# Performance work log

Hardware: AMD Instinct MI355X
Metric: run time of the kernel (lower is better)

Reference implementation:

```python
import jax, jax.numpy as jnp
import numpy as np

# ---- dims / hyperparams (match init_kwargs) ----
D, B, S, NE, NC = 256, 4, 8192, 2048, 512
WIN, RK, TKE, TKC = 4, 4, 4, 4          # s window, route_topk, expanded_topk, compressed_topk
ALPHA, BS2B, BB2S = 1.0, 0.5, 0.5       # alpha_b, beta_s_to_b, beta_b_to_s
S_SC, B_SC, X_SC = 0.25, 0.2, 0.15      # s/b/cross delta scales
EPS = 1e-5
INV_SQRT_D = float(1.0 / np.sqrt(D))


def _ln(x, g, b):
    m = jnp.mean(x, -1, keepdims=True)
    v = jnp.mean(jnp.square(x - m), -1, keepdims=True)
    return (x - m) * jax.lax.rsqrt(v + EPS) * g + b


def _window_prop(state, val, w):
    # local window attention via diagonal-bilinear pairwise scores; never builds [S,S]
    n = state.shape[1]
    offs = jnp.arange(-WIN, WIN + 1)
    idx = jnp.arange(n)[:, None] + offs[None, :]            # [n, K]
    valid = (idx >= 0) & (idx < n)
    idxc = jnp.clip(idx, 0, n - 1)
    nb_s = state[:, idxc]                                    # [B, n, K, D]
    nb_v = val[:, idxc]
    sc = jnp.einsum('bnd,bnkd->bnk', state * w, nb_s) * INV_SQRT_D
    sc = jnp.where(valid, sc, -1e30)
    a = jax.nn.softmax(sc, axis=-1)
    return (jnp.einsum('bnk,bnkd->bnd', a, nb_s),
            jnp.einsum('bnk,bnkd->bnd', a, nb_v))


def _topk_prop(state, val, w, k):
    # global topk sparse attention over the (small) expanded/compressed node set
    sc = jnp.einsum('bnd,bmd->bnm', state * w, state) * INV_SQRT_D
    top, idx = jax.lax.top_k(sc, k)                          # [B, N, k]
    a = jax.nn.softmax(top, axis=-1)
    take = jax.vmap(lambda x, i: x[i])                       # gather rows per batch
    nb_s = take(state, idx)                                  # [B, N, k, D]
    nb_v = take(val, idx)
    return (jnp.einsum('bnk,bnkd->bnd', a, nb_s),
            jnp.einsum('bnk,bnkd->bnd', a, nb_v))


def _sparse_transition(src_s, src_v, W, bias, nd, k):
    # LinearRoute logits -> topk dst per src -> softmax weights -> scatter-add into dst
    logits = src_s @ W + bias                                # [B, Ns, Nd]
    top, idx = jax.lax.top_k(logits, k)
    wgt = jax.nn.softmax(top, axis=-1)                       # [B, Ns, k]

    def scat(i, ww, fs, fv):
        ii = i.reshape(-1)
        cs = (ww[..., None] * fs[:, None, :]).reshape(-1, fs.shape[-1])
        cv = (ww[..., None] * fv[:, None, :]).reshape(-1, fv.shape[-1])
        z = jnp.zeros((nd, fs.shape[-1]), fs.dtype)
        return z.at[ii].add(cs), z.at[ii].add(cv)

    return jax.vmap(scat)(idx, wgt, src_s, src_v)            # [B, Nd, D] x2


def _forward(s_state, s_val, w_pair_s, w_pair_e, w_pair_c,
             W_expand, b_expand, W_b2s, b_b2s, W_comp, b_comp, W_s2b, b_s2b,
             ln_g_s, ln_b_s, ln_g_e, ln_b_e, ln_g_c, ln_b_c):
    bsz = s_state.shape[0]
    # 1) sequence window propagation + stabilize
    ds, dv = _window_prop(s_state, s_val, w_pair_s)
    s_state = jnp.tanh(s_state + S_SC * ds)
    s_val = _ln(s_val + S_SC * dv, ln_g_s, ln_b_s)
    # 2) compressed layer bootstrapped from zeros (compressed_b=None) + stabilize
    c_state = jnp.zeros((bsz, NC, D), s_state.dtype)
    c_val = _ln(jnp.zeros((bsz, NC, D), s_state.dtype), ln_g_c, ln_b_c)
    # 3) expanded layer: expand transition then topk propagation + stabilize
    e_state = jnp.zeros((bsz, NE, D), s_state.dtype)
    e_val = jnp.zeros((bsz, NE, D), s_state.dtype)
    sc_b = ALPHA * B_SC
    ds, dv = _sparse_transition(c_state, c_val, W_expand, b_expand, NE, RK)
    e_state = e_state + sc_b * ds; e_val = e_val + sc_b * dv
    ds, dv = _topk_prop(e_state, e_val, w_pair_e, TKE)
    e_state = jnp.tanh(e_state + sc_b * ds)
    e_val = _ln(e_val + sc_b * dv, ln_g_e, ln_b_e)
    # 4) expanded -> sequence cross update + stabilize
    sc_x = ALPHA * BB2S * X_SC
    ds, dv = _sparse_transition(e_state, e_val, W_b2s, b_b2s, S, RK)
    s_state = jnp.tanh(s_state + sc_x * ds)
    s_val = _ln(s_val + sc_x * dv, ln_g_s, ln_b_s)
    # 5) next compressed: compress, s->b, compressed propagation + stabilize
    nc_state, nc_val = c_state, c_val
    ds, dv = _sparse_transition(e_state, e_val, W_comp, b_comp, NC, RK)
    nc_state = nc_state + sc_b * ds; nc_val = nc_val + sc_b * dv
    sc_sb = ALPHA * BS2B * X_SC
    ds, dv = _sparse_transition(s_state, s_val, W_s2b, b_s2b, NC, RK)
    nc_state = nc_state + sc_sb * ds; nc_val = nc_val + sc_sb * dv
    ds, dv = _topk_prop(nc_state, nc_val, w_pair_c, TKC)
    nc_state = jnp.tanh(nc_state + sc_b * ds)
    nc_val = _ln(nc_val + sc_b * dv, ln_g_c, ln_b_c)
    return (s_state, s_val, nc_state, nc_val)


def setup_inputs() -> dict:
    key = jax.random.key(0)
    ks = jax.random.split(key, 16)
    rs = float(1.0 / np.sqrt(D))
    return {
        's_state': jax.random.normal(ks[0], (B, S, D), jnp.float32),
        's_val': jax.random.normal(ks[1], (B, S, D), jnp.float32),
        'w_pair_s': jax.random.normal(ks[2], (D,), jnp.float32) * rs,
        'w_pair_e': jax.random.normal(ks[3], (D,), jnp.float32) * rs,
        'w_pair_c': jax.random.normal(ks[4], (D,), jnp.float32) * rs,
        'W_expand': jax.random.normal(ks[5], (D, NE), jnp.float32) * rs,
        'b_expand': jnp.zeros((NE,), jnp.float32),
        'W_b2s': jax.random.normal(ks[6], (D, S), jnp.float32) * rs,
        'b_b2s': jnp.zeros((S,), jnp.float32),
        'W_comp': jax.random.normal(ks[7], (D, NC), jnp.float32) * rs,
        'b_comp': jnp.zeros((NC,), jnp.float32),
        'W_s2b': jax.random.normal(ks[8], (D, NC), jnp.float32) * rs,
        'b_s2b': jnp.zeros((NC,), jnp.float32),
        'ln_g_s': jnp.ones((D,), jnp.float32), 'ln_b_s': jnp.zeros((D,), jnp.float32),
        'ln_g_e': jnp.ones((D,), jnp.float32), 'ln_b_e': jnp.zeros((D,), jnp.float32),
        'ln_g_c': jnp.ones((D,), jnp.float32), 'ln_b_c': jnp.zeros((D,), jnp.float32),
    }


def reference(s_state, s_val, w_pair_s, w_pair_e, w_pair_c,
              W_expand, b_expand, W_b2s, b_b2s, W_comp, b_comp, W_s2b, b_s2b,
              ln_g_s, ln_b_s, ln_g_e, ln_b_e, ln_g_c, ln_b_c):
    return _forward(s_state, s_val, w_pair_s, w_pair_e, w_pair_c,
                    W_expand, b_expand, W_b2s, b_b2s, W_comp, b_comp, W_s2b, b_s2b,
                    ln_g_s, ln_b_s, ln_g_e, ln_b_e, ln_g_c, ln_b_c)
```

## Files before the change

kernel.cpp:

```cpp
#include <hip/hip_runtime.h>
#include <math.h>

#define DD 256
#define BATCH 4
#define SEQ 8192
#define NEE 2048
#define NCC 512
#define EPSL 1e-5f
#define INV_SQRT_D 0.0625f

typedef __attribute__((ext_vector_type(8))) short short8;
typedef __attribute__((ext_vector_type(4))) float f32x4;

__device__ __forceinline__ float4 ld4(const float* p){ return *(const float4*)p; }
__device__ __forceinline__ void st4(float* p, const float4& v){ *(float4*)p = v; }
__device__ __forceinline__ void fma4(float4& a, float s, const float4& b){
  a.x = fmaf(s,b.x,a.x); a.y = fmaf(s,b.y,a.y); a.z = fmaf(s,b.z,a.z); a.w = fmaf(s,b.w,a.w);
}
__device__ __forceinline__ float4 tanh4(const float4& v){
  float4 r; r.x=tanhf(v.x); r.y=tanhf(v.y); r.z=tanhf(v.z); r.w=tanhf(v.w); return r;
}
__device__ __forceinline__ ushort f2bf(float x){
  unsigned u = __float_as_uint(x);
  unsigned r = u + 0x7fffu + ((u >> 16) & 1u);
  return (ushort)(r >> 16);
}
__device__ __forceinline__ float bf2f(ushort h){
  return __uint_as_float(((unsigned)h) << 16);
}

__device__ __forceinline__ bool t4_better(float v1, int i1, float v2, int i2){
  return (v1 > v2) || (v1 == v2 && i1 < i2);
}
__device__ __forceinline__ void t4_init(float* v, int* i){
#pragma unroll
  for (int k=0;k<4;k++){ v[k] = -INFINITY; i[k] = 0x7fffffff; }
}
__device__ __forceinline__ void t4_insert(float* v, int* i, float nv, int ni){
  if (t4_better(nv, ni, v[3], i[3])){
    v[3]=nv; i[3]=ni;
    if (t4_better(v[3],i[3],v[2],i[2])){ float tv=v[2]; v[2]=v[3]; v[3]=tv; int ti=i[2]; i[2]=i[3]; i[3]=ti;
      if (t4_better(v[2],i[2],v[1],i[1])){ tv=v[1]; v[1]=v[2]; v[2]=tv; ti=i[1]; i[1]=i[2]; i[2]=ti;
        if (t4_better(v[1],i[1],v[0],i[0])){ tv=v[0]; v[0]=v[1]; v[1]=tv; ti=i[0]; i[0]=i[1]; i[1]=ti; }
      }
    }
  }
}
__device__ __forceinline__ void t4_ce(float* v, int* i, int x, int y){
  if (t4_better(v[y],i[y],v[x],i[x])){ float tv=v[x]; v[x]=v[y]; v[y]=tv; int ti=i[x]; i[x]=i[y]; i[y]=ti; }
}
__device__ __forceinline__ void t4_merge(float* av, int* ai, const float* bv, const int* bi){
  float lv[4]; int li[4];
#pragma unroll
  for (int k=0;k<4;k++){
    if (t4_better(av[k],ai[k],bv[3-k],bi[3-k])){ lv[k]=av[k]; li[k]=ai[k]; }
    else { lv[k]=bv[3-k]; li[k]=bi[3-k]; }
  }
  t4_ce(lv,li,0,2); t4_ce(lv,li,1,3); t4_ce(lv,li,0,1); t4_ce(lv,li,2,3);
#pragma unroll
  for (int k=0;k<4;k++){ av[k]=lv[k]; ai[k]=li[k]; }
}
__device__ __forceinline__ void t4_wave_merge(float* v, int* i){
#pragma unroll
  for (int off=1; off<64; off<<=1){
    float bv[4]; int bi[4];
#pragma unroll
    for (int k=0;k<4;k++){ bv[k]=__shfl_xor(v[k],off); bi[k]=__shfl_xor(i[k],off); }
    t4_merge(v,i,bv,bi);
  }
}

__global__ __launch_bounds__(256) void k0_prep(
    const float* __restrict__ b_expand, const float* __restrict__ b_b2s, const float* __restrict__ b_comp,
    const float* __restrict__ ln_b_c, const float* __restrict__ ln_g_e, const float* __restrict__ ln_b_e,
    float* __restrict__ sumE, int* __restrict__ idxB2S, float* __restrict__ wgtB2S,
    int* __restrict__ idxComp, float* __restrict__ wgtComp)
{
  __shared__ int s_idx[3][4];
  __shared__ float s_wgt[3][4];
  __shared__ float red[16];
  int t = threadIdx.x, wv = t>>6, lane = t&63;
  if (wv < 3){
    const float* arr = (wv==0)? b_expand : (wv==1? b_b2s : b_comp);
    int n = (wv==0)? NEE : (wv==1? SEQ : NCC);
    float v[4]; int ix[4]; t4_init(v,ix);
    for (int m=lane; m<n; m+=64) t4_insert(v,ix, arr[m], m);
    t4_wave_merge(v,ix);
    if (lane==0){
      float e0=1.f, e1=expf(v[1]-v[0]), e2=expf(v[2]-v[0]), e3=expf(v[3]-v[0]);
      float inv = 1.f/(e0+e1+e2+e3);
      s_idx[wv][0]=ix[0]; s_idx[wv][1]=ix[1]; s_idx[wv][2]=ix[2]; s_idx[wv][3]=ix[3];
      s_wgt[wv][0]=e0*inv; s_wgt[wv][1]=e1*inv; s_wgt[wv][2]=e2*inv; s_wgt[wv][3]=e3*inv;
    }
  }
  __syncthreads();
  float c = ln_b_c[t];
  float cs = c, cq = c*c;
#pragma unroll
  for (int off=32; off; off>>=1){ cs += __shfl_xor(cs,off); cq += __shfl_xor(cq,off); }
  if (lane==0){ red[wv]=cs; red[8+wv]=cq; }
  __syncthreads();
  float mean_c = (red[0]+red[1]+red[2]+red[3]) * (1.f/256.f);
  float var_c  = (red[8]+red[9]+red[10]+red[11]) * (1.f/256.f) - mean_c*mean_c;
  float cm = c - mean_c;
  float g = ln_g_e[t], be = ln_b_e[t];
  float a[4]; float q = 0.f;
#pragma unroll
  for (int k=0;k<4;k++){
    a[k] = 0.2f * (float)NCC * s_wgt[0][k];
    if (s_idx[0][k] < 4) q += a[k];
  }
  q *= 0.25f;
  float se = 0.f;
#pragma unroll
  for (int k=0;k<4;k++){
    float tk = a[k] + 0.2f*q;
    se += tk*cm*rsqrtf(tk*tk*var_c + EPSL)*g + be;
  }
  float tz = 0.2f*q;
  se += (float)(NEE-4) * (tz*cm*rsqrtf(tz*tz*var_c + EPSL)*g + be);
  sumE[t] = se;
  if (t < 4){
    idxB2S[t] = s_idx[1][t]; wgtB2S[t] = s_wgt[1][t];
    idxComp[t] = s_idx[2][t]; wgtComp[t] = s_wgt[2][t];
  }
}

__global__ __launch_bounds__(256) void k1_window(
    const float* __restrict__ s_state, const float* __restrict__ s_val,
    const float* __restrict__ w_pair_s, const float* __restrict__ ln_g_s, const float* __restrict__ ln_b_s,
    const float* __restrict__ sumE, const int* __restrict__ idxB2S, const float* __restrict__ wgtB2S,
    float* __restrict__ out_state, float* __restrict__ out_val)
{
  int gw = (blockIdx.x << 2) + (threadIdx.x >> 6);
  int lane = threadIdx.x & 63;
  int b = gw >> 13, r = gw & (SEQ-1);
  size_t rowoff = ((size_t)gw) << 8;
  size_t bbase = ((size_t)b) << 21;
  int d0 = lane << 2;
  float4 x = ld4(s_state + rowoff + d0);
  float4 v = ld4(s_val + rowoff + d0);
  float4 wp = ld4(w_pair_s + d0);
  float qx=x.x*wp.x, qy=x.y*wp.y, qz=x.z*wp.z, qw=x.w*wp.w;
  float sc[9]; float4 ns[9];
#pragma unroll
  for (int k=0;k<9;k++){
    int rr = r + k - 4;
    int rc = rr < 0 ? 0 : (rr > SEQ-1 ? SEQ-1 : rr);
    ns[k] = ld4(s_state + bbase + (((size_t)rc)<<8) + d0);
    sc[k] = qx*ns[k].x + qy*ns[k].y + qz*ns[k].z + qw*ns[k].w;
  }
#pragma unroll
  for (int off=32; off; off>>=1){
#pragma unroll
    for (int k=0;k<9;k++) sc[k] += __shfl_xor(sc[k], off);
  }
  float mx = -INFINITY;
#pragma unroll
  for (int k=0;k<9;k++){
    int rr = r + k - 4;
    sc[k] = (rr>=0 && rr<SEQ) ? sc[k]*INV_SQRT_D : -1e30f;
    mx = fmaxf(mx, sc[k]);
  }
  float ssum = 0.f;
#pragma unroll
  for (int k=0;k<9;k++){ sc[k] = expf(sc[k]-mx); ssum += sc[k]; }
  float inv = 1.f/ssum;
  float4 ds = make_float4(0,0,0,0), dv = make_float4(0,0,0,0);
#pragma unroll
  for (int k=0;k<9;k++) fma4(ds, sc[k]*inv, ns[k]);
#pragma unroll
  for (int k=0;k<9;k++){
    int rr = r + k - 4;
    int rc = rr < 0 ? 0 : (rr > SEQ-1 ? SEQ-1 : rr);
    float4 nv = ld4(s_val + bbase + (((size_t)rc)<<8) + d0);
    fma4(dv, sc[k]*inv, nv);
  }
  float4 s1;
  s1.x = tanhf(x.x + 0.25f*ds.x); s1.y = tanhf(x.y + 0.25f*ds.y);
  s1.z = tanhf(x.z + 0.25f*ds.z); s1.w = tanhf(x.w + 0.25f*ds.w);
  st4(out_state + rowoff + d0, tanh4(s1));
  float4 y;
  y.x = v.x + 0.25f*dv.x; y.y = v.y + 0.25f*dv.y; y.z = v.z + 0.25f*dv.z; y.w = v.w + 0.25f*dv.w;
  float sm = y.x+y.y+y.z+y.w;
  float sq = y.x*y.x+y.y*y.y+y.z*y.z+y.w*y.w;
#pragma unroll
  for (int off=32; off; off>>=1){ sm += __shfl_xor(sm,off); sq += __shfl_xor(sq,off); }
  float mean = sm*(1.f/256.f);
  float rstd = rsqrtf(sq*(1.f/256.f) - mean*mean + EPSL);
  float4 g = ld4(ln_g_s + d0), be = ld4(ln_b_s + d0);
  float4 y1;
  y1.x = (y.x-mean)*rstd*g.x + be.x; y1.y = (y.y-mean)*rstd*g.y + be.y;
  y1.z = (y.z-mean)*rstd*g.z + be.z; y1.w = (y.w-mean)*rstd*g.w + be.w;
#pragma unroll
  for (int k=0;k<4;k++){
    if (r == idxB2S[k]){
      float cb = 0.075f * wgtB2S[k];
      float4 sE = ld4(sumE + d0);
      fma4(y1, cb, sE);
    }
  }
  sm = y1.x+y1.y+y1.z+y1.w;
  sq = y1.x*y1.x+y1.y*y1.y+y1.z*y1.z+y1.w*y1.w;
#pragma unroll
  for (int off=32; off; off>>=1){ sm += __shfl_xor(sm,off); sq += __shfl_xor(sq,off); }
  float mean2 = sm*(1.f/256.f);
  float rstd2 = rsqrtf(sq*(1.f/256.f) - mean2*mean2 + EPSL);
  float4 o;
  o.x = (y1.x-mean2)*rstd2*g.x + be.x; o.y = (y1.y-mean2)*rstd2*g.y + be.y;
  o.z = (y1.z-mean2)*rstd2*g.z + be.z; o.w = (y1.w-mean2)*rstd2*g.w + be.w;
  st4(out_val + rowoff + d0, o);
}

__global__ __launch_bounds__(256) void k2w_pack(const float* __restrict__ W,
    ushort* __restrict__ Whi, ushort* __restrict__ Wlo)
{
  int t = blockIdx.x*256 + threadIdx.x;
  int kb = t >> 11;
  int cf = (t >> 6) & 31;
  int l  = t & 63;
  int k0 = kb*32 + ((l>>4)<<3);
  int col = (cf<<4) + (l&15);
  size_t off = (size_t)t << 3;
#pragma unroll
  for (int j=0;j<8;j++){
    float x = W[(size_t)(k0+j)*NCC + col];
    ushort h = f2bf(x);
    Whi[off+j] = h;
    Wlo[off+j] = f2bf(x - bf2f(h));
  }
}

__global__ __launch_bounds__(256, 4) void k2_mfma(
    const float* __restrict__ A, const ushort* __restrict__ Whi,
    const float* __restrict__ bias,
    int* __restrict__ topk_idx, float* __restrict__ topk_wgt, int* __restrict__ counts)
{
  __shared__ __align__(16) ushort Asp[2][32][264];
  __shared__ float mv[32][17];
  __shared__ int   mi[32][17];
  int tid = threadIdx.x;
  size_t row_base = (size_t)blockIdx.x * 32;
  int w = tid >> 6, l = tid & 63;
  int lg = l >> 4, lr = l & 15;
  const ushort* pw = Whi + ((w<<12) + (l<<3));

#define LOADG(KB, G, DST) { \
    const ushort* _p = pw + (KB)*16384 + (G)*1024; \
    DST[0] = *(const short8*)_p; \
    DST[2] = *(const short8*)(_p + 512); \
    DST[1] = *(const short8*)(_p + 131072); \
    DST[3] = *(const short8*)(_p + 131072 + 512); }

#define COMPG(G, B) { \
    int _c0 = (G)<<1, _c1 = _c0+1; \
    acc[0][_c0] = __builtin_amdgcn_mfma_f32_16x16x32_bf16(ah0, B[0], acc[0][_c0], 0,0,0); \
    acc[1][_c0] = __builtin_amdgcn_mfma_f32_16x16x32_bf16(ah1, B[0], acc[1][_c0], 0,0,0); \
    acc[0][_c1] = __builtin_amdgcn_mfma_f32_16x16x32_bf16(ah0, B[2], acc[0][_c1], 0,0,0); \
    acc[1][_c1] = __builtin_amdgcn_mfma_f32_16x16x32_bf16(ah1, B[2], acc[1][_c1], 0,0,0); \
    acc[0][_c0] = __builtin_amdgcn_mfma_f32_16x16x32_bf16(al0, B[0], acc[0][_c0], 0,0,0); \
    acc[1][_c0] = __builtin_amdgcn_mfma_f32_16x16x32_bf16(al1, B[0], acc[1][_c0], 0,0,0); \
    acc[0][_c0] = __builtin_amdgcn_mfma_f32_16x16x32_bf16(ah0, B[1], acc[0][_c0], 0,0,0); \
    acc[1][_c0] = __builtin_amdgcn_mfma_f32_16x16x32_bf16(ah1, B[1], acc[1][_c0], 0,0,0); \
    acc[0][_c1] = __builtin_amdgcn_mfma_f32_16x16x32_bf16(al0, B[2], acc[0][_c1], 0,0,0); \
    acc[1][_c1] = __builtin_amdgcn_mfma_f32_16x16x32_bf16(al1, B[2], acc[1][_c1], 0,0,0); \
    acc[0][_c1] = __builtin_amdgcn_mfma_f32_16x16x32_bf16(ah0, B[3], acc[0][_c1], 0,0,0); \
    acc[1][_c1] = __builtin_amdgcn_mfma_f32_16x16x32_bf16(ah1, B[3], acc[1][_c1], 0,0,0); }

  short8 bA[4], bB[4];
  LOADG(0, 0, bA);
  {
    const float4* Ab = (const float4*)(A + row_base*DD);
#pragma unroll
    for (int i=0;i<8;i++){
      int q = i*256 + tid;
      int row = q >> 6, k4 = q & 63;
      float4 x = Ab[q];
      ushort4 h, lo;
      h.x = f2bf(x.x); h.y = f2bf(x.y); h.z = f2bf(x.z); h.w = f2bf(x.w);
      lo.x = f2bf(x.x - bf2f(h.x)); lo.y = f2bf(x.y - bf2f(h.y));
      lo.z = f2bf(x.z - bf2f(h.z)); lo.w = f2bf(x.w - bf2f(h.w));
      *(ushort4*)&Asp[0][row][k4*4] = h;
      *(ushort4*)&Asp[1][row][k4*4] = lo;
    }
  }
  __syncthreads();
  f32x4 acc[2][8];
#pragma unroll
  for (int rf=0; rf<2; rf++)
#pragma unroll
    for (int cf=0; cf<8; cf++) acc[rf][cf] = (f32x4){0.f,0.f,0.f,0.f};
#pragma unroll 1
  for (int kb=0; kb<8; kb++){
    int ka = kb*32 + (lg<<3);
    short8 ah0 = *(const short8*)&Asp[0][lr][ka];
    short8 ah1 = *(const short8*)&Asp[0][16+lr][ka];
    short8 al0 = *(const short8*)&Asp[1][lr][ka];
    short8 al1 = *(const short8*)&Asp[1][16+lr][ka];
    LOADG(kb, 1, bB);
    __builtin_amdgcn_sched_barrier(0);
    COMPG(0, bA);
    LOADG(kb, 2, bA);
    __builtin_amdgcn_sched_barrier(0);
    COMPG(1, bB);
    LOADG(kb, 3, bB);
    __builtin_amdgcn_sched_barrier(0);
    COMPG(2, bA);
    if (kb < 7) LOADG(kb+1, 0, bA);
    __builtin_amdgcn_sched_barrier(0);
    COMPG(3, bB);
  }
#undef LOADG
#undef COMPG
  float bcol[8];
  int rel[8];
#pragma unroll
  for (int cf=0; cf<8; cf++){
    bcol[cf] = bias[(w<<7) + (cf<<4) + lr];
    rel[cf] = (cf<<4) + lr;
  }
#pragma unroll
  for (int rf=0; rf<2; rf++){
#pragma unroll
    for (int reg=0; reg<4; reg++){
      float av[8];
#pragma unroll
      for (int cf=0; cf<8; cf++) av[cf] = acc[rf][cf][reg] + bcol[cf];
      float tv4[4]; int tc4[4];
#pragma unroll
      for (int r=0; r<4; r++){
        float m = fmaxf(fmaxf(fmaxf(av[0],av[1]),fmaxf(av[2],av[3])),
                        fmaxf(fmaxf(av[4],av[5]),fmaxf(av[6],av[7])));
#pragma unroll
        for (int off=1; off<16; off<<=1) m = fmaxf(m, __shfl_xor(m, off));
        int cand = 0x7fffffff;
#pragma unroll
        for (int cf=7; cf>=0; cf--) cand = (av[cf]==m) ? rel[cf] : cand;
#pragma unroll
        for (int off=1; off<16; off<<=1) cand = min(cand, __shfl_xor(cand, off));
        tv4[r] = m; tc4[r] = cand;
        if (r < 3){
#pragma unroll
          for (int cf=0; cf<8; cf++) av[cf] = (rel[cf]==cand) ? -INFINITY : av[cf];
        }
      }
      if (lr == 0){
        int rowl = (rf<<4) + (lg<<2) + reg;
#pragma unroll
        for (int r=0; r<4; r++){ mv[rowl][(w<<2)+r] = tv4[r]; mi[rowl][(w<<2)+r] = (w<<7) + tc4[r]; }
      }
    }
  }
  __syncthreads();
  if (tid < 32){
    float v[4]; int ix[4]; t4_init(v, ix);
#pragma unroll
    for (int j=0; j<16; j++) t4_insert(v, ix, mv[tid][j], mi[tid][j]);
    float e0=1.f, e1=expf(v[1]-v[0]), e2=expf(v[2]-v[0]), e3=expf(v[3]-v[0]);
    float inv = 1.f/(e0+e1+e2+e3);
    size_t row = row_base + tid;
    int b = (int)(row >> 13);
    topk_idx[row*4+0]=ix[0]; topk_idx[row*4+1]=ix[1]; topk_idx[row*4+2]=ix[2]; topk_idx[row*4+3]=ix[3];
    topk_wgt[row*4+0]=e0*inv; topk_wgt[row*4+1]=e1*inv; topk_wgt[row*4+2]=e2*inv; topk_wgt[row*4+3]=e3*inv;
    atomicAdd(&counts[(b<<9)+ix[0]],1); atomicAdd(&counts[(b<<9)+ix[1]],1);
    atomicAdd(&counts[(b<<9)+ix[2]],1); atomicAdd(&counts[(b<<9)+ix[3]],1);
  }
}

__global__ void kz_zero(int* __restrict__ counts){
  int i = blockIdx.x*256 + threadIdx.x;
  if (i < BATCH*NCC) counts[i] = 0;
}

__global__ __launch_bounds__(256) void k3_scan(const int* __restrict__ counts,
    int* __restrict__ offsets, int* __restrict__ cursor)
{
  __shared__ int part[256];
  int t = threadIdx.x;
  int loc[8]; int s = 0;
#pragma unroll
  for (int i=0;i<8;i++){ loc[i] = counts[t*8+i]; s += loc[i]; }
  part[t] = s;
  __syncthreads();
  for (int off=1; off<256; off<<=1){
    int add = (t>=off)? part[t-off] : 0;
    __syncthreads();
    part[t] += add;
    __syncthreads();
  }
  int run = part[t] - s;
#pragma unroll
  for (int i=0;i<8;i++){ offsets[t*8+i] = run; cursor[t*8+i] = run; run += loc[i]; }
  if (t==255) offsets[BATCH*NCC] = run;
}

__global__ void k4_fill(const int* __restrict__ topk_idx, const float* __restrict__ topk_wgt,
    int* __restrict__ cursor, int* __restrict__ csr_src, float* __restrict__ csr_wgt)
{
  int row = blockIdx.x*256 + threadIdx.x;
  if (row >= BATCH*SEQ) return;
  int b = row >> 13, r = row & (SEQ-1);
#pragma unroll
  for (int k=0;k<4;k++){
    int dest = topk_idx[row*4+k];
    float wgt = topk_wgt[row*4+k];
    int pos = atomicAdd(&cursor[(b<<9)+dest], 1);
    csr_src[pos] = r;
    csr_wgt[pos] = 0.075f * wgt;
  }
}

__global__ __launch_bounds__(256) void k5_gather(
    const int* __restrict__ offsets, const int* __restrict__ csr_src, const float* __restrict__ csr_wgt,
    const float* __restrict__ st, const float* __restrict__ vl,
    const float* __restrict__ ln_b_c, const float* __restrict__ sumE,
    const int* __restrict__ idxComp, const float* __restrict__ wgtComp,
    float* __restrict__ ncs, float* __restrict__ ncv)
{
  int g = blockIdx.x;
  int b = g >> 9, dest = g & (NCC-1);
  int t = threadIdx.x;
  int i0 = offsets[g], i1 = offsets[g+1];
  const float* Sb = st + (((size_t)b)<<21);
  const float* Vb = vl + (((size_t)b)<<21);
  float accs = 0.f, accv = 0.f;
  for (int i=i0; i<i1; i++){
    int src = csr_src[i];
    float wg = csr_wgt[i];
    accs = fmaf(wg, Sb[((size_t)src<<8) + t], accs);
    accv = fmaf(wg, Vb[((size_t)src<<8) + t], accv);
  }
  float base = ln_b_c[t];
#pragma unroll
  for (int k=0;k<4;k++) if (dest == idxComp[k]) base = fmaf(0.2f*wgtComp[k], sumE[t], base);
  ncs[((size_t)g<<8) + t] = accs;
  ncv[((size_t)g<<8) + t] = base + accv;
}

__global__ __launch_bounds__(256) void k5t_transpose(const float* __restrict__ ncs, float* __restrict__ ncsT){
  __shared__ float tile[64][65];
  int b = blockIdx.z;
  int m0 = blockIdx.x*64, d0 = blockIdx.y*64;
  int tx = threadIdx.x & 63, ty = threadIdx.x >> 6;
  const float* src = ncs + (((size_t)b)<<17);
  for (int i=ty; i<64; i+=4) tile[i][tx] = src[(size_t)(m0+i)*DD + d0 + tx];
  __syncthreads();
  float* dst = ncsT + (((size_t)b)<<17);
  for (int i=ty; i<64; i+=4) dst[(size_t)(d0+i)*NCC + m0 + tx] = tile[tx][i];
}

__global__ __launch_bounds__(256) void k6_ncprop(
    const float* __restrict__ ncs, const float* __restrict__ ncv, const float* __restrict__ ncsT,
    const float* __restrict__ w_pair_c, const float* __restrict__ ln_g_c, const float* __restrict__ ln_b_c,
    float* __restrict__ o_ncs, float* __restrict__ o_ncv)
{
  __shared__ float Alds[256*13];
  int tid = threadIdx.x;
  int b = blockIdx.x >> 6;
  int n_base = (blockIdx.x & 63) << 3;
  const float* Sb = ncs + (((size_t)b)<<17);
  const float* Vb = ncv + (((size_t)b)<<17);
  const float* Tb = ncsT + (((size_t)b)<<17);
  float wc = w_pair_c[tid] * INV_SQRT_D;
#pragma unroll
  for (int i=0;i<8;i++) Alds[tid*13 + i] = Sb[(size_t)(n_base+i)*DD + tid] * wc;
  __syncthreads();
  int lane = tid & 63, rg = tid >> 6;
  int r0 = rg << 1, c0 = lane << 3;
  float acc[2][8];
#pragma unroll
  for (int j=0;j<2;j++)
#pragma unroll
    for (int c=0;c<8;c++) acc[j][c] = 0.f;
  for (int kk=0; kk<256; kk++){
    float4 w0 = ld4(Tb + (size_t)kk*NCC + c0);
    float4 w1 = ld4(Tb + (size_t)kk*NCC + c0 + 4);
    float a0 = Alds[kk*13 + r0];
    float a1 = Alds[kk*13 + r0 + 1];
    float wv_[8] = {w0.x,w0.y,w0.z,w0.w,w1.x,w1.y,w1.z,w1.w};
#pragma unroll
    for (int c=0;c<8;c++){
      acc[0][c] = fmaf(a0, wv_[c], acc[0][c]);
      acc[1][c] = fmaf(a1, wv_[c], acc[1][c]);
    }
  }
  int d0 = lane << 2;
  float4 g4 = ld4(ln_g_c + d0), be4 = ld4(ln_b_c + d0);
#pragma unroll
  for (int j=0;j<2;j++){
    float tv[4]; int ti[4]; t4_init(tv,ti);
#pragma unroll
    for (int c=0;c<8;c++) t4_insert(tv,ti, acc[j][c], c0+c);
    t4_wave_merge(tv,ti);
    float e0=1.f, e1=expf(tv[1]-tv[0]), e2=expf(tv[2]-tv[0]), e3=expf(tv[3]-tv[0]);
    float inv = 1.f/(e0+e1+e2+e3);
    float aw[4] = {e0*inv, e1*inv, e2*inv, e3*inv};
    int n = n_base + r0 + j;
    float4 stt = ld4(Sb + (size_t)n*DD + d0);
    float4 vv  = ld4(Vb + (size_t)n*DD + d0);
    float4 dsv = make_float4(0,0,0,0), dvv = make_float4(0,0,0,0);
#pragma unroll
    for (int k=0;k<4;k++){
      float4 ms = ld4(Sb + (size_t)ti[k]*DD + d0);
      float4 mv = ld4(Vb + (size_t)ti[k]*DD + d0);
      fma4(dsv, aw[k], ms); fma4(dvv, aw[k], mv);
    }
    float4 os;
    os.x = tanhf(stt.x + 0.2f*dsv.x); os.y = tanhf(stt.y + 0.2f*dsv.y);
    os.z = tanhf(stt.z + 0.2f*dsv.z); os.w = tanhf(stt.w + 0.2f*dsv.w);
    size_t orow = (((size_t)b)<<17) + ((size_t)n<<8);
    st4(o_ncs + orow + d0, os);
    float4 y;
    y.x = vv.x + 0.2f*dvv.x; y.y = vv.y + 0.2f*dvv.y;
    y.z = vv.z + 0.2f*dvv.z; y.w = vv.w + 0.2f*dvv.w;
    float sm = y.x+y.y+y.z+y.w;
    float sq = y.x*y.x+y.y*y.y+y.z*y.z+y.w*y.w;
#pragma unroll
    for (int off=32; off; off>>=1){ sm += __shfl_xor(sm,off); sq += __shfl_xor(sq,off); }
    float mean = sm*(1.f/256.f);
    float rstd = rsqrtf(sq*(1.f/256.f) - mean*mean + EPSL);
    float4 o;
    o.x = (y.x-mean)*rstd*g4.x + be4.x; o.y = (y.y-mean)*rstd*g4.y + be4.y;
    o.z = (y.z-mean)*rstd*g4.z + be4.z; o.w = (y.w-mean)*rstd*g4.w + be4.w;
    st4(o_ncv + orow + d0, o);
  }
}

extern "C" void kernel_launch(void* const* d_in, const int* in_sizes, int n_in,
                              void* d_out, int out_size, void* d_ws, size_t ws_size,
                              hipStream_t stream)
{
  const float* s_state = (const float*)d_in[0];
  const float* s_val   = (const float*)d_in[1];
  const float* w_pair_s= (const float*)d_in[2];
  const float* w_pair_c= (const float*)d_in[4];
  const float* b_expand= (const float*)d_in[6];
  const float* b_b2s   = (const float*)d_in[8];
  const float* b_comp  = (const float*)d_in[10];
  const float* W_s2b   = (const float*)d_in[11];
  const float* b_s2b   = (const float*)d_in[12];
  const float* ln_g_s  = (const float*)d_in[13];
  const float* ln_b_s  = (const float*)d_in[14];
  const float* ln_g_e  = (const float*)d_in[15];
  const float* ln_b_e  = (const float*)d_in[16];
  const float* ln_g_c  = (const float*)d_in[17];
  const float* ln_b_c  = (const float*)d_in[18];

  float* o_sstate = (float*)d_out;
  float* o_sval   = o_sstate + (size_t)BATCH*SEQ*DD;
  float* o_ncs    = o_sval + (size_t)BATCH*SEQ*DD;
  float* o_ncv    = o_ncs + (size_t)BATCH*NCC*DD;

  char* w = (char*)d_ws;
  float* sumE    = (float*)(w);
  int*   idxB2S  = (int*)(w + 1024);
  float* wgtB2S  = (float*)(w + 1040);
  int*   idxComp = (int*)(w + 1056);
  float* wgtComp = (float*)(w + 1072);
  int*   topk_idx= (int*)(w + 4096);
  float* topk_wgt= (float*)(w + 4096 + 524288);
  int*   counts  = (int*)(w + 1052672);
  int*   offsets = (int*)(w + 1069056);
  int*   cursor  = (int*)(w + 1085440);
  int*   csr_src = (int*)(w + 1101824);
  float* csr_wgt = (float*)(w + 1626112);
  float* ncs_ws  = (float*)(w + 2150400);
  float* ncv_ws  = ncs_ws + (size_t)BATCH*NCC*DD;
  float* ncsT_ws = ncv_ws + (size_t)BATCH*NCC*DD;
  ushort* wpk_hi = (ushort*)(w + 8441856);
  ushort* wpk_lo = (ushort*)(w + 8441856 + 262144);

  hipLaunchKernelGGL(k0_prep, dim3(1), dim3(256), 0, stream,
      b_expand, b_b2s, b_comp, ln_b_c, ln_g_e, ln_b_e, sumE, idxB2S, wgtB2S, idxComp, wgtComp);
  hipLaunchKernelGGL(k2w_pack, dim3(64), dim3(256), 0, stream, W_s2b, wpk_hi, wpk_lo);
  hipLaunchKernelGGL(k1_window, dim3(8192), dim3(256), 0, stream,
      s_state, s_val, w_pair_s, ln_g_s, ln_b_s, sumE, idxB2S, wgtB2S, o_sstate, o_sval);
  hipLaunchKernelGGL(kz_zero, dim3(8), dim3(256), 0, stream, counts);
  hipLaunchKernelGGL(k2_mfma, dim3(1024), dim3(256), 0, stream,
      o_sstate, wpk_hi, b_s2b, topk_idx, topk_wgt, counts);
  hipLaunchKernelGGL(k3_scan, dim3(1), dim3(256), 0, stream, counts, offsets, cursor);
  hipLaunchKernelGGL(k4_fill, dim3(128), dim3(256), 0, stream,
      topk_idx, topk_wgt, cursor, csr_src, csr_wgt);
  hipLaunchKernelGGL(k5_gather, dim3(2048), dim3(256), 0, stream,
      offsets, csr_src, csr_wgt, o_sstate, o_sval, ln_b_c, sumE, idxComp, wgtComp, ncs_ws, ncv_ws);
  hipLaunchKernelGGL(k5t_transpose, dim3(8,4,BATCH), dim3(256), 0, stream, ncs_ws, ncsT_ws);
  hipLaunchKernelGGL(k6_ncprop, dim3(256), dim3(256), 0, stream,
      ncs_ws, ncv_ws, ncsT_ws, w_pair_c, ln_g_c, ln_b_c, o_ncs, o_ncv);
}
```

Before: 420.0 us.

## Split CSR gather across two blocks per destination with atomic accumulation

The gather kernel now launches two blocks per compressed destination, each handling half of the source list, and adds partial sums into pre-initialized buffers with float atomics. A new init kernel zeroes the accumulators, writes the bias base and zeroes the counts, replacing the old zero kernel. The inner loop is unrolled by four with independent accumulators so more gathered loads are in flight. This targets load imbalance and latency in the gather, at the cost of an extra init pass, atomic traffic and nondeterministic summation order.

```diff
diff --git a/kernel.cpp b/kernel.cpp
--- a/kernel.cpp
+++ b/kernel.cpp
@@ -123,6 +123,26 @@
   if (t < 4){
     idxB2S[t] = s_idx[1][t]; wgtB2S[t] = s_wgt[1][t];
     idxComp[t] = s_idx[2][t]; wgtComp[t] = s_wgt[2][t];
+  }
+}
+
+__global__ __launch_bounds__(256) void kz_init(int* __restrict__ counts,
+    float* __restrict__ ncs, float* __restrict__ ncv,
+    const float* __restrict__ ln_b_c, const float* __restrict__ sumE,
+    const int* __restrict__ idxComp, const float* __restrict__ wgtComp)
+{
+  int bid = blockIdx.x;
+  int t = threadIdx.x;
+  if (bid < BATCH*NCC){
+    int dest = bid & (NCC-1);
+    float base = ln_b_c[t];
+#pragma unroll
+    for (int k=0;k<4;k++) if (dest == idxComp[k]) base = fmaf(0.2f*wgtComp[k], sumE[t], base);
+    ncs[((size_t)bid<<8) + t] = 0.f;
+    ncv[((size_t)bid<<8) + t] = base;
+  } else {
+    int i = (bid - BATCH*NCC)*256 + t;
+    if (i < BATCH*NCC) counts[i] = 0;
   }
 }
 
@@ -367,11 +387,6 @@
   }
 }
 
-__global__ void kz_zero(int* __restrict__ counts){
-  int i = blockIdx.x*256 + threadIdx.x;
-  if (i < BATCH*NCC) counts[i] = 0;
-}
-
 __global__ __launch_bounds__(256) void k3_scan(const int* __restrict__ counts,
     int* __restrict__ offsets, int* __restrict__ cursor)
 {
@@ -413,28 +428,45 @@
 __global__ __launch_bounds__(256) void k5_gather(
     const int* __restrict__ offsets, const int* __restrict__ csr_src, const float* __restrict__ csr_wgt,
     const float* __restrict__ st, const float* __restrict__ vl,
-    const float* __restrict__ ln_b_c, const float* __restrict__ sumE,
-    const int* __restrict__ idxComp, const float* __restrict__ wgtComp,
     float* __restrict__ ncs, float* __restrict__ ncv)
 {
-  int g = blockIdx.x;
-  int b = g >> 9, dest = g & (NCC-1);
+  int g2 = blockIdx.x;
+  int g  = g2 >> 1;
+  int half = g2 & 1;
+  int b = g >> 9;
   int t = threadIdx.x;
   int i0 = offsets[g], i1 = offsets[g+1];
+  int n = i1 - i0;
+  int ia = i0 + ((n * half) >> 1);
+  int ib = i0 + ((n * (half+1)) >> 1);
+  if (ia >= ib) return;
   const float* Sb = st + (((size_t)b)<<21);
   const float* Vb = vl + (((size_t)b)<<21);
-  float accs = 0.f, accv = 0.f;
-  for (int i=i0; i<i1; i++){
+  float as0=0.f, as1=0.f, as2=0.f, as3=0.f;
+  float av0=0.f, av1=0.f, av2=0.f, av3=0.f;
+  int i = ia;
+  for (; i+3 < ib; i += 4){
+    int s0 = csr_src[i],   s1 = csr_src[i+1], s2 = csr_src[i+2], s3 = csr_src[i+3];
+    float w0 = csr_wgt[i], w1 = csr_wgt[i+1], w2 = csr_wgt[i+2], w3 = csr_wgt[i+3];
+    float x0 = Sb[((size_t)s0<<8)+t], y0 = Vb[((size_t)s0<<8)+t];
+    float x1 = Sb[((size_t)s1<<8)+t], y1 = Vb[((size_t)s1<<8)+t];
+    float x2 = Sb[((size_t)s2<<8)+t], y2 = Vb[((size_t)s2<<8)+t];
+    float x3 = Sb[((size_t)s3<<8)+t], y3 = Vb[((size_t)s3<<8)+t];
+    as0 = fmaf(w0,x0,as0); av0 = fmaf(w0,y0,av0);
+    as1 = fmaf(w1,x1,as1); av1 = fmaf(w1,y1,av1);
+    as2 = fmaf(w2,x2,as2); av2 = fmaf(w2,y2,av2);
+    as3 = fmaf(w3,x3,as3); av3 = fmaf(w3,y3,av3);
+  }
+  for (; i < ib; i++){
     int src = csr_src[i];
     float wg = csr_wgt[i];
-    accs = fmaf(wg, Sb[((size_t)src<<8) + t], accs);
-    accv = fmaf(wg, Vb[((size_t)src<<8) + t], accv);
-  }
-  float base = ln_b_c[t];
-#pragma unroll
-  for (int k=0;k<4;k++) if (dest == idxComp[k]) base = fmaf(0.2f*wgtComp[k], sumE[t], base);
-  ncs[((size_t)g<<8) + t] = accs;
-  ncv[((size_t)g<<8) + t] = base + accv;
+    as0 = fmaf(wg, Sb[((size_t)src<<8)+t], as0);
+    av0 = fmaf(wg, Vb[((size_t)src<<8)+t], av0);
+  }
+  float accs = (as0+as1)+(as2+as3);
+  float accv = (av0+av1)+(av2+av3);
+  atomicAdd(&ncs[((size_t)g<<8) + t], accs);
+  atomicAdd(&ncv[((size_t)g<<8) + t], accv);
 }
 
 __global__ __launch_bounds__(256) void k5t_transpose(const float* __restrict__ ncs, float* __restrict__ ncsT){
@@ -572,17 +604,18 @@
 
   hipLaunchKernelGGL(k0_prep, dim3(1), dim3(256), 0, stream,
       b_expand, b_b2s, b_comp, ln_b_c, ln_g_e, ln_b_e, sumE, idxB2S, wgtB2S, idxComp, wgtComp);
+  hipLaunchKernelGGL(kz_init, dim3(BATCH*NCC + 8), dim3(256), 0, stream,
+      counts, ncs_ws, ncv_ws, ln_b_c, sumE, idxComp, wgtComp);
   hipLaunchKernelGGL(k2w_pack, dim3(64), dim3(256), 0, stream, W_s2b, wpk_hi, wpk_lo);
   hipLaunchKernelGGL(k1_window, dim3(8192), dim3(256), 0, stream,
       s_state, s_val, w_pair_s, ln_g_s, ln_b_s, sumE, idxB2S, wgtB2S, o_sstate, o_sval);
-  hipLaunchKernelGGL(kz_zero, dim3(8), dim3(256), 0, stream, counts);
   hipLaunchKernelGGL(k2_mfma, dim3(1024), dim3(256), 0, stream,
       o_sstate, wpk_hi, b_s2b, topk_idx, topk_wgt, counts);
   hipLaunchKernelGGL(k3_scan, dim3(1), dim3(256), 0, stream, counts, offsets, cursor);
   hipLaunchKernelGGL(k4_fill, dim3(128), dim3(256), 0, stream,
       topk_idx, topk_wgt, cursor, csr_src, csr_wgt);
-  hipLaunchKernelGGL(k5_gather, dim3(2048), dim3(256), 0, stream,
-      offsets, csr_src, csr_wgt, o_sstate, o_sval, ln_b_c, sumE, idxComp, wgtComp, ncs_ws, ncv_ws);
+  hipLaunchKernelGGL(k5_gather, dim3(4096), dim3(256), 0, stream,
+      offsets, csr_src, csr_wgt, o_sstate, o_sval, ncs_ws, ncv_ws);
   hipLaunchKernelGGL(k5t_transpose, dim3(8,4,BATCH), dim3(256), 0, stream, ncs_ws, ncsT_ws);
   hipLaunchKernelGGL(k6_ncprop, dim3(256), dim3(256), 0, stream,
       ncs_ws, ncv_ws, ncsT_ws, w_pair_c, ln_g_c, ln_b_c, o_ncs, o_ncv);
```

After: 399.7 us. 1.05x faster.
